# Kernel optimization log

Measured on AMD Instinct MI355X. Metric: run time of the kernel, lower is better.

The kernel has to match this reference:

```python
import jax, jax.numpy as jnp
import numpy as np

B, S, D = 16, 16, 4096
H, KV, HD = 32, 8, 128
MAX_B, MAX_S = 16, 4096
START = 4080


def setup_inputs() -> dict:
    key = jax.random.key(0)
    ks = jax.random.split(key, 10)
    sc = 0.02
    # RoPE angles for positions [START, START+S)
    inv_freq = 1.0 / (10000.0 ** (np.arange(0, HD, 2, dtype=np.float32) / HD))  # [HD/2]
    pos = np.arange(START, START + S, dtype=np.float32)
    ang = np.outer(pos, inv_freq)  # [S, HD/2]
    return {
        'x': jax.random.normal(ks[0], (B, S, D), jnp.float32),
        'k': jax.random.normal(ks[1], (B, S, D), jnp.float32),
        'v': jax.random.normal(ks[2], (B, S, D), jnp.float32),
        'wq': jax.random.normal(ks[3], (D, H * HD), jnp.float32) * sc,
        'wk': jax.random.normal(ks[4], (D, KV * HD), jnp.float32) * sc,
        'wv': jax.random.normal(ks[5], (D, KV * HD), jnp.float32) * sc,
        'wo': jax.random.normal(ks[6], (H * HD, D), jnp.float32) * sc,
        'cache_k': jax.random.normal(ks[7], (MAX_B, MAX_S, KV, HD), jnp.float32),
        'cache_v': jax.random.normal(ks[8], (MAX_B, MAX_S, KV, HD), jnp.float32),
        'freqs_cos': jnp.asarray(np.cos(ang)),
        'freqs_sin': jnp.asarray(np.sin(ang)),
        'start_pos': START,
    }


def _rope(t, cos, sin):
    # t: [B,S,nh,HD]; interleaved complex pairs (even=real, odd=imag)
    t2 = t.reshape(*t.shape[:-1], HD // 2, 2)
    x0, x1 = t2[..., 0], t2[..., 1]
    c = cos[None, :, None, :]
    s = sin[None, :, None, :]
    r0 = x0 * c - x1 * s
    r1 = x0 * s + x1 * c
    return jnp.stack([r0, r1], axis=-1).reshape(t.shape)


def reference(x, k, v, wq, wk, wv, wo, cache_k, cache_v, freqs_cos, freqs_sin, start_pos):
    rep = H // KV
    xq = (x @ wq).reshape(B, S, H, HD)
    xk = (k @ wk).reshape(B, S, KV, HD)
    xv = (v @ wv).reshape(B, S, KV, HD)
    xq = _rope(xq, freqs_cos, freqs_sin)
    xk = _rope(xk, freqs_cos, freqs_sin)
    # KV-cache append (start_pos is a static Python int)
    cache_k = jax.lax.dynamic_update_slice(cache_k, xk, (0, start_pos, 0, 0))
    cache_v = jax.lax.dynamic_update_slice(cache_v, xv, (0, start_pos, 0, 0))
    T = start_pos + S
    keys = cache_k[:B, :T]    # [B,T,KV,HD]
    values = cache_v[:B, :T]  # [B,T,KV,HD]
    # GQA without materializing repeat_kv: q head h = g*rep + r
    q = xq.reshape(B, S, KV, rep, HD)
    scores = jnp.einsum('bsgrd,btgd->bgrst', q, keys) / jnp.sqrt(jnp.float32(HD))
    attn = jax.nn.softmax(scores.astype(jnp.float32), axis=-1).astype(q.dtype)
    out = jnp.einsum('bgrst,btgd->bsgrd', attn, values).reshape(B, S, H * HD)
    return out @ wo
```

## Files before the change

kernel.cpp:

```cpp
#include <hip/hip_runtime.h>

typedef __attribute__((ext_vector_type(8))) short bf8_t;
typedef __attribute__((ext_vector_type(4))) short s4_t;
typedef __attribute__((ext_vector_type(4))) float f4_t;

#define DEV static __device__ __forceinline__

DEV short f2bf(float f) {
  union { float f; unsigned u; } x; x.f = f;
  unsigned r = x.u + 0x7FFFu + ((x.u >> 16) & 1u);
  return (short)(r >> 16);
}
DEV float bf2f(short h) {
  union { unsigned u; float f; } x; x.u = ((unsigned)(unsigned short)h) << 16;
  return x.f;
}
DEV f4_t mfma16(bf8_t a, bf8_t b, f4_t c) {
  return __builtin_amdgcn_mfma_f32_16x16x32_bf16(a, b, c, 0, 0, 0);
}
DEV f4_t zf4() { f4_t v = {0.f, 0.f, 0.f, 0.f}; return v; }

DEV void cvt8(const f4_t& f0, const f4_t& f1, bf8_t& hv, bf8_t& lv) {
#pragma unroll
  for (int i = 0; i < 4; i++) {
    short h = f2bf(f0[i]); hv[i] = h; lv[i] = f2bf(f0[i] - bf2f(h));
  }
#pragma unroll
  for (int i = 0; i < 4; i++) {
    short h = f2bf(f1[i]); hv[4 + i] = h; lv[4 + i] = f2bf(f1[i] - bf2f(h));
  }
}

__global__ __launch_bounds__(256, 4)
void qkv_kernel(const float* __restrict__ x, const float* __restrict__ kin,
                const float* __restrict__ vin, const float* __restrict__ wq,
                const float* __restrict__ wk, const float* __restrict__ wv,
                float* __restrict__ part)
{
  __shared__ short Bh[2][64][40], Bl[2][64][40];

  int bid = blockIdx.x;
  int sw = (bid & 7) * 192 + (bid >> 3);
  int ks = sw / 384;
  int r  = sw % 384;

  int lin, N, cbase;
  const float* A; const float* W;
  if (r < 256)      { lin = r;       A = x;   W = wq; N = 4096; cbase = 0; }
  else if (r < 320) { lin = r - 256; A = kin; W = wk; N = 1024; cbase = 4096; }
  else              { lin = r - 320; A = vin; W = wv; N = 1024; cbase = 5120; }
  int m0 = (lin & 3) * 64;
  int n0 = (lin >> 2) * 64;
  int k0 = ks * 1024;

  int tid = threadIdx.x, w = tid >> 6, l = tid & 63;
  f4_t acc[4];
#pragma unroll
  for (int i = 0; i < 4; i++) acc[i] = zf4();

  int bn = tid & 63;
  int bch = (tid >> 6) ^ ((tid >> 3) & 3);
  int bk = bch * 8;
  const float* wptr = W + n0 + bn;

  const float* afrag = A + (m0 + w * 16 + (l & 15)) * 4096 + k0 + (l >> 4) * 8;

  f4_t a0 = *(const f4_t*)afrag;
  f4_t a1 = *(const f4_t*)(afrag + 4);
  float br[8];
#pragma unroll
  for (int j = 0; j < 8; j++) br[j] = wptr[(size_t)(k0 + bk + j) * N];

  for (int it = 0; it < 32; ++it) {
    int cur = it & 1;
    {
      f4_t f0, f1;
#pragma unroll
      for (int j = 0; j < 4; j++) { f0[j] = br[j]; f1[j] = br[4 + j]; }
      bf8_t hv, lv; cvt8(f0, f1, hv, lv);
      *(bf8_t*)&Bh[cur][bn][bk] = hv;
      *(bf8_t*)&Bl[cur][bn][bk] = lv;
    }
    f4_t a0c = a0, a1c = a1;
    if (it + 1 < 32) {
      a0 = *(const f4_t*)(afrag + (it + 1) * 32);
      a1 = *(const f4_t*)(afrag + (it + 1) * 32 + 4);
#pragma unroll
      for (int j = 0; j < 8; j++)
        br[j] = wptr[(size_t)(k0 + (it + 1) * 32 + bk + j) * N];
    }
    __syncthreads();
    bf8_t ah, al; cvt8(a0c, a1c, ah, al);
    __builtin_amdgcn_s_setprio(1);
#pragma unroll
    for (int nt = 0; nt < 4; ++nt) {
      bf8_t bh = *(const bf8_t*)&Bh[cur][nt * 16 + (l & 15)][(l >> 4) * 8];
      bf8_t bl = *(const bf8_t*)&Bl[cur][nt * 16 + (l & 15)][(l >> 4) * 8];
      acc[nt] = mfma16(ah, bh, acc[nt]);
      acc[nt] = mfma16(ah, bl, acc[nt]);
      acc[nt] = mfma16(al, bh, acc[nt]);
    }
    __builtin_amdgcn_s_setprio(0);
  }

  float* po = part + ((size_t)ks * 256 + m0) * 6144 + cbase + n0;
  int cl = l & 15, gq = l >> 4;
#pragma unroll
  for (int nt = 0; nt < 4; ++nt)
#pragma unroll
    for (int i = 0; i < 4; i++)
      po[(w * 16 + gq * 4 + i) * 6144 + nt * 16 + cl] = acc[nt][i];
}

__global__ __launch_bounds__(256)
void reduce_rope(const float* __restrict__ part,
                 const float* __restrict__ fcos, const float* __restrict__ fsin,
                 short* __restrict__ qh, short* __restrict__ ql,
                 short* __restrict__ kh, short* __restrict__ vb)
{
  int gid = blockIdx.x * 256 + threadIdx.x;
  int row = gid / 768;
  int c8  = (gid - row * 768) * 8;
  const float* p = part + (size_t)row * 6144 + c8;
  float v[8];
#pragma unroll
  for (int j = 0; j < 8; j++) v[j] = p[j];
#pragma unroll
  for (int ksp = 1; ksp < 4; ksp++) {
    const float* q = p + (size_t)ksp * 256 * 6144;
#pragma unroll
    for (int j = 0; j < 8; j++) v[j] += q[j];
  }
  int s = row & 15, bb = row >> 4;
  if (c8 < 4096) {
    int h = c8 >> 7, d = c8 & 127;
    f4_t c  = *(const f4_t*)(fcos + s * 64 + (d >> 1));
    f4_t sn = *(const f4_t*)(fsin + s * 64 + (d >> 1));
    bf8_t hv, lv;
#pragma unroll
    for (int pr = 0; pr < 4; pr++) {
      float x0 = v[2 * pr], x1 = v[2 * pr + 1];
      float r0 = (x0 * c[pr] - x1 * sn[pr]) * 0.08838834764831845f;
      float r1 = (x0 * sn[pr] + x1 * c[pr]) * 0.08838834764831845f;
      short h0 = f2bf(r0); hv[2 * pr] = h0; lv[2 * pr] = f2bf(r0 - bf2f(h0));
      short h1 = f2bf(r1); hv[2 * pr + 1] = h1; lv[2 * pr + 1] = f2bf(r1 - bf2f(h1));
    }
    int idx = ((bb * 8 + (h >> 2)) * 64 + (h & 3) * 16 + s) * 128 + d;
    *(bf8_t*)(qh + idx) = hv;
    *(bf8_t*)(ql + idx) = lv;
  } else if (c8 < 5120) {
    int cc = c8 - 4096; int h = cc >> 7, d = cc & 127;
    f4_t c  = *(const f4_t*)(fcos + s * 64 + (d >> 1));
    f4_t sn = *(const f4_t*)(fsin + s * 64 + (d >> 1));
    bf8_t hv;
#pragma unroll
    for (int pr = 0; pr < 4; pr++) {
      float x0 = v[2 * pr], x1 = v[2 * pr + 1];
      float r0 = x0 * c[pr] - x1 * sn[pr];
      float r1 = x0 * sn[pr] + x1 * c[pr];
      hv[2 * pr]     = f2bf(r0);
      hv[2 * pr + 1] = f2bf(r1);
    }
    int idx = ((bb * 8 + h) * 16 + s) * 128 + d;
    *(bf8_t*)(kh + idx) = hv;
  } else {
    int cc = c8 - 5120; int h = cc >> 7, d = cc & 127;
    bf8_t hv;
#pragma unroll
    for (int j = 0; j < 8; j++) hv[j] = f2bf(v[j]);
    int idx = ((bb * 8 + h) * 16 + s) * 128 + d;
    *(bf8_t*)(vb + idx) = hv;
  }
}

__global__ __launch_bounds__(256, 3)
void attn_kernel(const float* __restrict__ ck, const float* __restrict__ cv,
                 const short* __restrict__ qhp, const short* __restrict__ qlp,
                 const short* __restrict__ khp, const short* __restrict__ vbp,
                 const int* __restrict__ startp,
                 float* __restrict__ Op, float* __restrict__ mp,
                 float* __restrict__ lp)
{
  __shared__ short Kh[64][136];
  __shared__ short Vs[64][130];
  __shared__ short Ps[4][16][72];

  int bid = blockIdx.x;
  int bg = bid >> 3, sp = bid & 7;
  int b = bg >> 3, g = bg & 7;
  int tid = threadIdx.x, w = tid >> 6, l = tid & 63;
  int start = *startp;

  bf8_t qfh[4], qfl[4];
  {
    int qoff = (bg * 64 + w * 16 + (l & 15)) * 128 + (l >> 4) * 8;
#pragma unroll
    for (int kt = 0; kt < 4; ++kt) {
      qfh[kt] = *(const bf8_t*)(qhp + qoff + kt * 32);
      qfl[kt] = *(const bf8_t*)(qlp + qoff + kt * 32);
    }
  }
  f4_t of[8];
#pragma unroll
  for (int i = 0; i < 8; i++) of[i] = zf4();
  float mrun[4], lrun[4];
#pragma unroll
  for (int i = 0; i < 4; i++) { mrun[i] = -1e30f; lrun[i] = 0.f; }

  int srow = tid >> 2, sdc = (tid & 3) * 32;

  for (int tile = 0; tile < 8; ++tile) {
    int tb = sp * 512 + tile * 64;
    int t = tb + srow;
    __syncthreads();
    {
      if (t >= start) {
        const short* sh = khp + ((bg * 16) + (t - start)) * 128 + sdc;
#pragma unroll
        for (int j = 0; j < 4; j++)
          *(bf8_t*)&Kh[srow][sdc + 8 * j] = *(const bf8_t*)(sh + 8 * j);
      } else {
        const float* src = ck + (((size_t)b * 4096 + t) * 8 + g) * 128 + sdc;
#pragma unroll
        for (int j = 0; j < 4; j++) {
          f4_t f0 = *(const f4_t*)(src + 8 * j);
          f4_t f1 = *(const f4_t*)(src + 8 * j + 4);
          bf8_t hv;
#pragma unroll
          for (int i = 0; i < 4; i++) { hv[i] = f2bf(f0[i]); hv[4 + i] = f2bf(f1[i]); }
          *(bf8_t*)&Kh[srow][sdc + 8 * j] = hv;
        }
      }
    }
    {
      unsigned* vdst = (unsigned*)&Vs[srow][sdc];
      if (t >= start) {
        const short* sv = vbp + ((bg * 16) + (t - start)) * 128 + sdc;
#pragma unroll
        for (int j = 0; j < 4; j++) {
          bf8_t vv = *(const bf8_t*)(sv + 8 * j);
          union { bf8_t v; unsigned u[4]; } cu; cu.v = vv;
#pragma unroll
          for (int q = 0; q < 4; q++) vdst[4 * j + q] = cu.u[q];
        }
      } else {
        const float* src = cv + (((size_t)b * 4096 + t) * 8 + g) * 128 + sdc;
#pragma unroll
        for (int j = 0; j < 4; j++) {
          f4_t f0 = *(const f4_t*)(src + 8 * j);
          f4_t f1 = *(const f4_t*)(src + 8 * j + 4);
#pragma unroll
          for (int q = 0; q < 2; q++)
            vdst[4 * j + q] = (unsigned)(unsigned short)f2bf(f0[2 * q]) |
                              ((unsigned)(unsigned short)f2bf(f0[2 * q + 1]) << 16);
#pragma unroll
          for (int q = 0; q < 2; q++)
            vdst[4 * j + 2 + q] = (unsigned)(unsigned short)f2bf(f1[2 * q]) |
                                  ((unsigned)(unsigned short)f2bf(f1[2 * q + 1]) << 16);
        }
      }
    }
    __syncthreads();

    f4_t sf[4];
#pragma unroll
    for (int i = 0; i < 4; i++) sf[i] = zf4();
    __builtin_amdgcn_s_setprio(1);
#pragma unroll
    for (int tt = 0; tt < 4; ++tt) {
#pragma unroll
      for (int kt = 0; kt < 4; ++kt) {
        bf8_t kb = *(const bf8_t*)&Kh[tt * 16 + (l & 15)][kt * 32 + (l >> 4) * 8];
        sf[tt] = mfma16(qfh[kt], kb, sf[tt]);
        sf[tt] = mfma16(qfl[kt], kb, sf[tt]);
      }
    }
    __builtin_amdgcn_s_setprio(0);

    float mt[4];
#pragma unroll
    for (int i = 0; i < 4; i++)
      mt[i] = fmaxf(fmaxf(sf[0][i], sf[1][i]), fmaxf(sf[2][i], sf[3][i]));
#pragma unroll
    for (int st = 1; st < 16; st <<= 1)
#pragma unroll
      for (int i = 0; i < 4; i++) mt[i] = fmaxf(mt[i], __shfl_xor(mt[i], st));
    float sc[4];
#pragma unroll
    for (int i = 0; i < 4; i++) {
      float mn = fmaxf(mrun[i], mt[i]);
      sc[i] = __expf(mrun[i] - mn);
      mrun[i] = mn;
    }
    float rs[4] = {0.f, 0.f, 0.f, 0.f};
#pragma unroll
    for (int tt = 0; tt < 4; ++tt)
#pragma unroll
      for (int i = 0; i < 4; i++) {
        float pexp = __expf(sf[tt][i] - mrun[i]);
        rs[i] += pexp;
        Ps[w][(l >> 4) * 4 + i][tt * 16 + (l & 15)] = f2bf(pexp);
      }
#pragma unroll
    for (int st = 1; st < 16; st <<= 1)
#pragma unroll
      for (int i = 0; i < 4; i++) rs[i] += __shfl_xor(rs[i], st);
#pragma unroll
    for (int i = 0; i < 4; i++) lrun[i] = lrun[i] * sc[i] + rs[i];
#pragma unroll
    for (int dt = 0; dt < 8; ++dt)
#pragma unroll
      for (int i = 0; i < 4; i++) of[dt][i] *= sc[i];

    __builtin_amdgcn_s_setprio(1);
#pragma unroll
    for (int kt2 = 0; kt2 < 2; ++kt2) {
      bf8_t pa = *(const bf8_t*)&Ps[w][l & 15][kt2 * 32 + (l >> 4) * 8];
      int trow = kt2 * 32 + (l >> 4) * 8;
#pragma unroll
      for (int dt = 0; dt < 8; ++dt) {
        int dcol = dt * 16 + (l & 15);
        bf8_t vf;
#pragma unroll
        for (int e = 0; e < 8; ++e) vf[e] = Vs[trow + e][dcol];
        of[dt] = mfma16(pa, vf, of[dt]);
      }
    }
    __builtin_amdgcn_s_setprio(0);
  }

  size_t obase = ((size_t)(bg * 8 + sp) * 64 + w * 16) * 128;
#pragma unroll
  for (int dt = 0; dt < 8; ++dt)
#pragma unroll
    for (int i = 0; i < 4; i++)
      Op[obase + ((l >> 4) * 4 + i) * 128 + dt * 16 + (l & 15)] = of[dt][i];
  if ((l & 15) == 0) {
    int rbase = (bg * 8 + sp) * 64 + w * 16 + (l >> 4) * 4;
#pragma unroll
    for (int i = 0; i < 4; i++) { mp[rbase + i] = mrun[i]; lp[rbase + i] = lrun[i]; }
  }
}

__global__ __launch_bounds__(256)
void merge_kernel(const float* __restrict__ Op, const float* __restrict__ mp,
                  const float* __restrict__ lp, short* __restrict__ attnb)
{
  int bg = blockIdx.x;
  int tid = threadIdx.x;
  int row = tid >> 2, dc = (tid & 3) * 32;
  int b = bg >> 3, g = bg & 7;
  int r = row >> 4, s = row & 15;
  float mm[8], ww[8];
  float M = -1e30f;
#pragma unroll
  for (int spp = 0; spp < 8; ++spp) {
    mm[spp] = mp[(bg * 8 + spp) * 64 + row];
    M = fmaxf(M, mm[spp]);
  }
  float denom = 0.f;
#pragma unroll
  for (int spp = 0; spp < 8; ++spp) {
    ww[spp] = __expf(mm[spp] - M);
    denom += lp[(bg * 8 + spp) * 64 + row] * ww[spp];
  }
  float inv = 1.0f / denom;
  int ob = (b * 16 + s) * 4096 + (g * 4 + r) * 128 + dc;
#pragma unroll
  for (int j = 0; j < 8; j++) {
    f4_t a = zf4();
#pragma unroll
    for (int spp = 0; spp < 8; ++spp) {
      f4_t o = *(const f4_t*)(Op + ((size_t)(bg * 8 + spp) * 64 + row) * 128 + dc + j * 4);
#pragma unroll
      for (int i = 0; i < 4; i++) a[i] += ww[spp] * o[i];
    }
    s4_t o4;
#pragma unroll
    for (int i = 0; i < 4; i++) o4[i] = f2bf(a[i] * inv);
    *(s4_t*)(attnb + ob + j * 4) = o4;
  }
}

__global__ __launch_bounds__(256, 4)
void wo_kernel(const short* __restrict__ attnb, const float* __restrict__ wo,
               float* __restrict__ wpart)
{
  __shared__ short Bs[2][64][40];

  int bid = blockIdx.x;
  int sw = (bid & 7) * 128 + (bid >> 3);
  int ks = sw >> 8, r = sw & 255;
  int m0 = (r & 3) * 64, n0 = (r >> 2) * 64, k0 = ks * 1024;

  int tid = threadIdx.x, w = tid >> 6, l = tid & 63;
  f4_t acc[4];
#pragma unroll
  for (int i = 0; i < 4; i++) acc[i] = zf4();

  int bn = tid & 63;
  int bch = (tid >> 6) ^ ((tid >> 3) & 3);
  int bk = bch * 8;
  const float* wptr = wo + n0 + bn;
  const short* afrag = attnb + (m0 + w * 16 + (l & 15)) * 4096 + k0 + (l >> 4) * 8;

  bf8_t areg = *(const bf8_t*)afrag;
  float br[8];
#pragma unroll
  for (int j = 0; j < 8; j++) br[j] = wptr[(size_t)(k0 + bk + j) * 4096];

  for (int it = 0; it < 32; ++it) {
    int cur = it & 1;
    {
      bf8_t hv;
#pragma unroll
      for (int j = 0; j < 8; j++) hv[j] = f2bf(br[j]);
      *(bf8_t*)&Bs[cur][bn][bk] = hv;
    }
    bf8_t ac = areg;
    if (it + 1 < 32) {
      areg = *(const bf8_t*)(afrag + (it + 1) * 32);
#pragma unroll
      for (int j = 0; j < 8; j++)
        br[j] = wptr[(size_t)(k0 + (it + 1) * 32 + bk + j) * 4096];
    }
    __syncthreads();
    __builtin_amdgcn_s_setprio(1);
#pragma unroll
    for (int nt = 0; nt < 4; ++nt) {
      bf8_t bb_ = *(const bf8_t*)&Bs[cur][nt * 16 + (l & 15)][(l >> 4) * 8];
      acc[nt] = mfma16(ac, bb_, acc[nt]);
    }
    __builtin_amdgcn_s_setprio(0);
  }

  float* po = wpart + ((size_t)ks * 256 + m0) * 4096 + n0;
  int cl = l & 15, gq = l >> 4;
#pragma unroll
  for (int nt = 0; nt < 4; ++nt)
#pragma unroll
    for (int i = 0; i < 4; i++)
      po[(w * 16 + gq * 4 + i) * 4096 + nt * 16 + cl] = acc[nt][i];
}

__global__ __launch_bounds__(256)
void reduce_out(const float* __restrict__ wpart, float* __restrict__ out)
{
  int gid = blockIdx.x * 256 + threadIdx.x;
  size_t idx4 = (size_t)gid * 4;
  f4_t s = *(const f4_t*)(wpart + idx4);
#pragma unroll
  for (int ksp = 1; ksp < 4; ksp++) {
    f4_t t = *(const f4_t*)(wpart + (size_t)ksp * 1048576 + idx4);
#pragma unroll
    for (int i = 0; i < 4; i++) s[i] += t[i];
  }
  *(f4_t*)(out + idx4) = s;
}

extern "C" void kernel_launch(void* const* d_in, const int* in_sizes, int n_in,
                              void* d_out, int out_size, void* d_ws, size_t ws_size,
                              hipStream_t stream)
{
  const float* x  = (const float*)d_in[0];
  const float* k  = (const float*)d_in[1];
  const float* v  = (const float*)d_in[2];
  const float* wq = (const float*)d_in[3];
  const float* wk = (const float*)d_in[4];
  const float* wv = (const float*)d_in[5];
  const float* wo = (const float*)d_in[6];
  const float* ck = (const float*)d_in[7];
  const float* cv = (const float*)d_in[8];
  const float* fc = (const float*)d_in[9];
  const float* fs = (const float*)d_in[10];
  const int*   spv = (const int*)d_in[11];
  float* out = (float*)d_out;

  char* p = (char*)d_ws;
  float* S = (float*)p; p += (size_t)34 * 1024 * 1024;
  float* qpart = S;
  float* Oppp  = S;
  float* wpart = S;
  short* qh = (short*)p; p += (size_t)128 * 64 * 128 * 2;
  short* ql = (short*)p; p += (size_t)128 * 64 * 128 * 2;
  short* kh = (short*)p; p += (size_t)128 * 16 * 128 * 2;
  short* vb = (short*)p; p += (size_t)128 * 16 * 128 * 2;
  short* attnb = (short*)p; p += (size_t)256 * 4096 * 2;
  float* mp = (float*)p; p += (size_t)1024 * 64 * 4;
  float* lp = (float*)p; p += (size_t)1024 * 64 * 4;

  hipLaunchKernelGGL(qkv_kernel, dim3(1536), dim3(256), 0, stream,
                     x, k, v, wq, wk, wv, qpart);
  hipLaunchKernelGGL(reduce_rope, dim3(768), dim3(256), 0, stream,
                     qpart, fc, fs, qh, ql, kh, vb);
  hipLaunchKernelGGL(attn_kernel, dim3(1024), dim3(256), 0, stream,
                     ck, cv, qh, ql, kh, vb, spv, Oppp, mp, lp);
  hipLaunchKernelGGL(merge_kernel, dim3(128), dim3(256), 0, stream,
                     Oppp, mp, lp, attnb);
  hipLaunchKernelGGL(wo_kernel, dim3(1024), dim3(256), 0, stream,
                     attnb, wo, wpart);
  hipLaunchKernelGGL(reduce_out, dim3(1024), dim3(256), 0, stream,
                     wpart, out);
}
```

Baseline: 293.4 us.

## Register-prefetch KV tiles and store V transposed in LDS for attention

The attention kernel now processes 32-key tiles and prefetches the next tile's K/V fp32 data into registers (ISSUE) while computing the current tile, then converts and writes it to LDS (WRITE). V is transposed through cross-lane shuffles so the PV MFMA operand is a single vector LDS read instead of eight strided scalar reads. The new K/V rows are now kept as fp32 in cache layout, so both cache and fresh rows share one load path. This adds shuffle work, twice as many tile iterations and barriers, and higher register pressure.

```diff
diff --git a/kernel.cpp b/kernel.cpp
--- a/kernel.cpp
+++ b/kernel.cpp
@@ -3,6 +3,7 @@
 typedef __attribute__((ext_vector_type(8))) short bf8_t;
 typedef __attribute__((ext_vector_type(4))) short s4_t;
 typedef __attribute__((ext_vector_type(4))) float f4_t;
+typedef __attribute__((ext_vector_type(4))) unsigned u4_t;
 
 #define DEV static __device__ __forceinline__
 
@@ -14,6 +15,10 @@
 DEV float bf2f(short h) {
   union { unsigned u; float f; } x; x.u = ((unsigned)(unsigned short)h) << 16;
   return x.f;
+}
+DEV unsigned pk2(float a, float b) {
+  return (unsigned)(unsigned short)f2bf(a) |
+         ((unsigned)(unsigned short)f2bf(b) << 16);
 }
 DEV f4_t mfma16(bf8_t a, bf8_t b, f4_t c) {
   return __builtin_amdgcn_mfma_f32_16x16x32_bf16(a, b, c, 0, 0, 0);
@@ -116,7 +121,7 @@
 void reduce_rope(const float* __restrict__ part,
                  const float* __restrict__ fcos, const float* __restrict__ fsin,
                  short* __restrict__ qh, short* __restrict__ ql,
-                 short* __restrict__ kh, short* __restrict__ vb)
+                 float* __restrict__ kf, float* __restrict__ vf)
 {
   int gid = blockIdx.x * 256 + threadIdx.x;
   int row = gid / 768;
@@ -152,38 +157,44 @@
     int cc = c8 - 4096; int h = cc >> 7, d = cc & 127;
     f4_t c  = *(const f4_t*)(fcos + s * 64 + (d >> 1));
     f4_t sn = *(const f4_t*)(fsin + s * 64 + (d >> 1));
-    bf8_t hv;
-#pragma unroll
-    for (int pr = 0; pr < 4; pr++) {
+    f4_t o0, o1;
+#pragma unroll
+    for (int pr = 0; pr < 2; pr++) {
       float x0 = v[2 * pr], x1 = v[2 * pr + 1];
-      float r0 = x0 * c[pr] - x1 * sn[pr];
-      float r1 = x0 * sn[pr] + x1 * c[pr];
-      hv[2 * pr]     = f2bf(r0);
-      hv[2 * pr + 1] = f2bf(r1);
-    }
-    int idx = ((bb * 8 + h) * 16 + s) * 128 + d;
-    *(bf8_t*)(kh + idx) = hv;
+      o0[2 * pr]     = x0 * c[pr] - x1 * sn[pr];
+      o0[2 * pr + 1] = x0 * sn[pr] + x1 * c[pr];
+    }
+#pragma unroll
+    for (int pr = 2; pr < 4; pr++) {
+      float x0 = v[2 * pr], x1 = v[2 * pr + 1];
+      o1[2 * (pr - 2)]     = x0 * c[pr] - x1 * sn[pr];
+      o1[2 * (pr - 2) + 1] = x0 * sn[pr] + x1 * c[pr];
+    }
+    size_t idx = (((size_t)bb * 16 + s) * 8 + h) * 128 + d;
+    *(f4_t*)(kf + idx) = o0;
+    *(f4_t*)(kf + idx + 4) = o1;
   } else {
     int cc = c8 - 5120; int h = cc >> 7, d = cc & 127;
-    bf8_t hv;
-#pragma unroll
-    for (int j = 0; j < 8; j++) hv[j] = f2bf(v[j]);
-    int idx = ((bb * 8 + h) * 16 + s) * 128 + d;
-    *(bf8_t*)(vb + idx) = hv;
+    size_t idx = (((size_t)bb * 16 + s) * 8 + h) * 128 + d;
+    f4_t o0, o1;
+#pragma unroll
+    for (int j = 0; j < 4; j++) { o0[j] = v[j]; o1[j] = v[4 + j]; }
+    *(f4_t*)(vf + idx) = o0;
+    *(f4_t*)(vf + idx + 4) = o1;
   }
 }
 
 __global__ __launch_bounds__(256, 3)
 void attn_kernel(const float* __restrict__ ck, const float* __restrict__ cv,
                  const short* __restrict__ qhp, const short* __restrict__ qlp,
-                 const short* __restrict__ khp, const short* __restrict__ vbp,
+                 const float* __restrict__ kfp, const float* __restrict__ vfp,
                  const int* __restrict__ startp,
                  float* __restrict__ Op, float* __restrict__ mp,
                  float* __restrict__ lp)
 {
-  __shared__ short Kh[64][136];
-  __shared__ short Vs[64][130];
-  __shared__ short Ps[4][16][72];
+  __shared__ short Kh[32][136];
+  __shared__ short Vt[128][40];
+  __shared__ short Ps[4][16][40];
 
   int bid = blockIdx.x;
   int bg = bid >> 3, sp = bid & 7;
@@ -207,80 +218,84 @@
 #pragma unroll
   for (int i = 0; i < 4; i++) { mrun[i] = -1e30f; lrun[i] = 0.f; }
 
-  int srow = tid >> 2, sdc = (tid & 3) * 32;
-
-  for (int tile = 0; tile < 8; ++tile) {
-    int tb = sp * 512 + tile * 64;
-    int t = tb + srow;
-    __syncthreads();
-    {
-      if (t >= start) {
-        const short* sh = khp + ((bg * 16) + (t - start)) * 128 + sdc;
-#pragma unroll
-        for (int j = 0; j < 4; j++)
-          *(bf8_t*)&Kh[srow][sdc + 8 * j] = *(const bf8_t*)(sh + 8 * j);
-      } else {
-        const float* src = ck + (((size_t)b * 4096 + t) * 8 + g) * 128 + sdc;
-#pragma unroll
-        for (int j = 0; j < 4; j++) {
-          f4_t f0 = *(const f4_t*)(src + 8 * j);
-          f4_t f1 = *(const f4_t*)(src + 8 * j + 4);
-          bf8_t hv;
-#pragma unroll
-          for (int i = 0; i < 4; i++) { hv[i] = f2bf(f0[i]); hv[4 + i] = f2bf(f1[i]); }
-          *(bf8_t*)&Kh[srow][sdc + 8 * j] = hv;
-        }
+  int st_t = tid >> 3;
+  int d0   = (tid & 7) * 16;
+  int rr   = (tid >> 3) & 7;
+  int oo   = tid >> 6;
+
+  f4_t kr[4], vr[4];
+
+  auto ISSUE = [&](int tile) {
+    int t = sp * 512 + tile * 32 + st_t;
+    size_t o_st = (((size_t)b * 4096 + t) * 8 + g) * 128;
+    size_t o_fr = (((size_t)b * 16 + (size_t)(t - start)) * 8 + g) * 128;
+    const float* kp_ = (t < start) ? (ck + o_st) : (kfp + o_fr);
+    const float* vp_ = (t < start) ? (cv + o_st) : (vfp + o_fr);
+#pragma unroll
+    for (int j = 0; j < 4; j++) kr[j] = *(const f4_t*)(kp_ + d0 + 4 * j);
+#pragma unroll
+    for (int j = 0; j < 4; j++) vr[j] = *(const f4_t*)(vp_ + d0 + 4 * j);
+  };
+
+  auto WRITE = [&]() {
+    unsigned kp[8];
+#pragma unroll
+    for (int p = 0; p < 8; p++)
+      kp[p] = pk2(kr[p >> 1][(p & 1) * 2], kr[p >> 1][(p & 1) * 2 + 1]);
+    u4_t kw0 = {kp[0], kp[1], kp[2], kp[3]};
+    u4_t kw1 = {kp[4], kp[5], kp[6], kp[7]};
+    *(u4_t*)&Kh[st_t][d0] = kw0;
+    *(u4_t*)&Kh[st_t][d0 + 8] = kw1;
+
+    unsigned vp[8];
+#pragma unroll
+    for (int p = 0; p < 8; p++)
+      vp[p] = pk2(vr[p >> 1][(p & 1) * 2], vr[p >> 1][(p & 1) * 2 + 1]);
+#pragma unroll
+    for (int kk = 1; kk < 8; kk <<= 1) {
+      unsigned nv[8];
+#pragma unroll
+      for (int i = 0; i < 8; i++) {
+        unsigned ex = __shfl_xor(vp[i ^ kk], kk * 8);
+        bool sw = (((i & kk) != 0) != ((rr & kk) != 0));
+        nv[i] = sw ? ex : vp[i];
       }
-    }
-    {
-      unsigned* vdst = (unsigned*)&Vs[srow][sdc];
-      if (t >= start) {
-        const short* sv = vbp + ((bg * 16) + (t - start)) * 128 + sdc;
-#pragma unroll
-        for (int j = 0; j < 4; j++) {
-          bf8_t vv = *(const bf8_t*)(sv + 8 * j);
-          union { bf8_t v; unsigned u[4]; } cu; cu.v = vv;
-#pragma unroll
-          for (int q = 0; q < 4; q++) vdst[4 * j + q] = cu.u[q];
-        }
-      } else {
-        const float* src = cv + (((size_t)b * 4096 + t) * 8 + g) * 128 + sdc;
-#pragma unroll
-        for (int j = 0; j < 4; j++) {
-          f4_t f0 = *(const f4_t*)(src + 8 * j);
-          f4_t f1 = *(const f4_t*)(src + 8 * j + 4);
-#pragma unroll
-          for (int q = 0; q < 2; q++)
-            vdst[4 * j + q] = (unsigned)(unsigned short)f2bf(f0[2 * q]) |
-                              ((unsigned)(unsigned short)f2bf(f0[2 * q + 1]) << 16);
-#pragma unroll
-          for (int q = 0; q < 2; q++)
-            vdst[4 * j + 2 + q] = (unsigned)(unsigned short)f2bf(f1[2 * q]) |
-                                  ((unsigned)(unsigned short)f2bf(f1[2 * q + 1]) << 16);
-        }
-      }
-    }
-    __syncthreads();
-
-    f4_t sf[4];
-#pragma unroll
-    for (int i = 0; i < 4; i++) sf[i] = zf4();
+#pragma unroll
+      for (int i = 0; i < 8; i++) vp[i] = nv[i];
+    }
+    u4_t ra, rb;
+#pragma unroll
+    for (int i = 0; i < 4; i++) {
+      ra[i] = (vp[2 * i] & 0xffffu) | (vp[2 * i + 1] << 16);
+      rb[i] = (vp[2 * i] >> 16) | (vp[2 * i + 1] & 0xffff0000u);
+    }
+    *(u4_t*)&Vt[d0 + 2 * rr][oo * 8] = ra;
+    *(u4_t*)&Vt[d0 + 2 * rr + 1][oo * 8] = rb;
+  };
+
+  ISSUE(0);
+  WRITE();
+  __syncthreads();
+  ISSUE(1);
+
+  for (int tile = 0; tile < 16; ++tile) {
+    f4_t sf[2];
+#pragma unroll
+    for (int i = 0; i < 2; i++) sf[i] = zf4();
     __builtin_amdgcn_s_setprio(1);
 #pragma unroll
-    for (int tt = 0; tt < 4; ++tt) {
+    for (int tt = 0; tt < 2; ++tt)
 #pragma unroll
       for (int kt = 0; kt < 4; ++kt) {
         bf8_t kb = *(const bf8_t*)&Kh[tt * 16 + (l & 15)][kt * 32 + (l >> 4) * 8];
         sf[tt] = mfma16(qfh[kt], kb, sf[tt]);
         sf[tt] = mfma16(qfl[kt], kb, sf[tt]);
       }
-    }
     __builtin_amdgcn_s_setprio(0);
 
     float mt[4];
 #pragma unroll
-    for (int i = 0; i < 4; i++)
-      mt[i] = fmaxf(fmaxf(sf[0][i], sf[1][i]), fmaxf(sf[2][i], sf[3][i]));
+    for (int i = 0; i < 4; i++) mt[i] = fmaxf(sf[0][i], sf[1][i]);
 #pragma unroll
     for (int st = 1; st < 16; st <<= 1)
 #pragma unroll
@@ -294,7 +309,7 @@
     }
     float rs[4] = {0.f, 0.f, 0.f, 0.f};
 #pragma unroll
-    for (int tt = 0; tt < 4; ++tt)
+    for (int tt = 0; tt < 2; ++tt)
 #pragma unroll
       for (int i = 0; i < 4; i++) {
         float pexp = __expf(sf[tt][i] - mrun[i]);
@@ -313,20 +328,22 @@
       for (int i = 0; i < 4; i++) of[dt][i] *= sc[i];
 
     __builtin_amdgcn_s_setprio(1);
-#pragma unroll
-    for (int kt2 = 0; kt2 < 2; ++kt2) {
-      bf8_t pa = *(const bf8_t*)&Ps[w][l & 15][kt2 * 32 + (l >> 4) * 8];
-      int trow = kt2 * 32 + (l >> 4) * 8;
+    {
+      bf8_t pa = *(const bf8_t*)&Ps[w][l & 15][(l >> 4) * 8];
 #pragma unroll
       for (int dt = 0; dt < 8; ++dt) {
-        int dcol = dt * 16 + (l & 15);
-        bf8_t vf;
-#pragma unroll
-        for (int e = 0; e < 8; ++e) vf[e] = Vs[trow + e][dcol];
-        of[dt] = mfma16(pa, vf, of[dt]);
+        bf8_t vfr = *(const bf8_t*)&Vt[dt * 16 + (l & 15)][(l >> 4) * 8];
+        of[dt] = mfma16(pa, vfr, of[dt]);
       }
     }
     __builtin_amdgcn_s_setprio(0);
+
+    if (tile < 15) {
+      __syncthreads();
+      WRITE();
+      __syncthreads();
+      if (tile < 14) ISSUE(tile + 2);
+    }
   }
 
   size_t obase = ((size_t)(bg * 8 + sp) * 64 + w * 16) * 128;
@@ -483,8 +500,8 @@
   float* wpart = S;
   short* qh = (short*)p; p += (size_t)128 * 64 * 128 * 2;
   short* ql = (short*)p; p += (size_t)128 * 64 * 128 * 2;
-  short* kh = (short*)p; p += (size_t)128 * 16 * 128 * 2;
-  short* vb = (short*)p; p += (size_t)128 * 16 * 128 * 2;
+  float* kf = (float*)p; p += (size_t)256 * 8 * 128 * 4;
+  float* vf = (float*)p; p += (size_t)256 * 8 * 128 * 4;
   short* attnb = (short*)p; p += (size_t)256 * 4096 * 2;
   float* mp = (float*)p; p += (size_t)1024 * 64 * 4;
   float* lp = (float*)p; p += (size_t)1024 * 64 * 4;
@@ -492,9 +509,9 @@
   hipLaunchKernelGGL(qkv_kernel, dim3(1536), dim3(256), 0, stream,
                      x, k, v, wq, wk, wv, qpart);
   hipLaunchKernelGGL(reduce_rope, dim3(768), dim3(256), 0, stream,
-                     qpart, fc, fs, qh, ql, kh, vb);
+                     qpart, fc, fs, qh, ql, kf, vf);
   hipLaunchKernelGGL(attn_kernel, dim3(1024), dim3(256), 0, stream,
-                     ck, cv, qh, ql, kh, vb, spv, Oppp, mp, lp);
+                     ck, cv, qh, ql, kf, vf, spv, Oppp, mp, lp);
   hipLaunchKernelGGL(merge_kernel, dim3(128), dim3(256), 0, stream,
                      Oppp, mp, lp, attnb);
   hipLaunchKernelGGL(wo_kernel, dim3(1024), dim3(256), 0, stream,
```

Result: no change. 290.0 us (-1.2%).
